# Performance work log

Measured on AMD Instinct MI355X. Metric: run time of the kernel, lower is better.

## Reference

```python
import jax, jax.numpy as jnp
import numpy as np

IN_DIM = 3
OUT_DIM = 3
HIDDEN = [40, 40, 40, 40, 40, 40]
N_POINTS = 2_097_152


def _glorot(key, fan_in, fan_out):
    std = jnp.sqrt(2.0 / (fan_in + fan_out)).astype(jnp.float32)
    return jax.random.normal(key, (fan_in, fan_out), dtype=jnp.float32) * std


def setup_inputs() -> dict:
    key = jax.random.key(0)
    keys = jax.random.split(key, 8)
    coords = jax.random.uniform(keys[0], (N_POINTS, IN_DIM), dtype=jnp.float32)
    dims = [IN_DIM] + HIDDEN + [OUT_DIM]  # [3,40,40,40,40,40,40,3]
    inp = {"coords": coords}
    for i in range(7):
        inp[f"W{i}"] = _glorot(keys[i + 1], dims[i], dims[i + 1])
        inp[f"b{i}"] = jnp.zeros((dims[i + 1],), dtype=jnp.float32)
    return inp


def reference(coords, W0, b0, W1, b1, W2, b2, W3, b3, W4, b4, W5, b5, W6, b6):
    # 7-layer coordinate MLP: Linear+Tanh x6, final Linear. coords: [N,3] -> [N,3]
    Ws = [W0, W1, W2, W3, W4, W5, W6]
    bs = [b0, b1, b2, b3, b4, b5, b6]
    x = coords
    for i in range(6):
        x = jnp.tanh(x @ Ws[i] + bs[i])
    return x @ Ws[6] + bs[6]
```

## Files before the change

kernel.cpp:

```cpp
#include <hip/hip_runtime.h>


typedef _Float16 f16x8 __attribute__((ext_vector_type(8)));
typedef float    f32x16 __attribute__((ext_vector_type(16)));
typedef unsigned int u32x4 __attribute__((ext_vector_type(4)));

#define NFRAG  35
#define TABN   385
#define TABREP 8
#define TABH   0.025f
#define INVH   40.0f
#define TABR   4.8f
#define UOFF   192.0f
#define UMAX   383.999f

__constant__ int INV[48] = {
     0,  1,  2,  3,   8,  9, 10, 11,   4,  5,  6,  7,  12, 13, 14, 15,
    16, 17, 18, 19,  24, 25, 26, 27,  20, 21, 22, 23,  28, 29, 30, 31,
    32, 33, 34, 35,  -1, -1, -1, -1,  36, 37, 38, 39,  -2, -3, -1, -1 };

__global__ void prep_frags(const float* __restrict__ W0, const float* __restrict__ b0,
                           const float* __restrict__ W1, const float* __restrict__ b1,
                           const float* __restrict__ W2, const float* __restrict__ b2,
                           const float* __restrict__ W3, const float* __restrict__ b3,
                           const float* __restrict__ W4, const float* __restrict__ b4,
                           const float* __restrict__ W5, const float* __restrict__ b5,
                           const float* __restrict__ W6, const float* __restrict__ b6,
                           unsigned short* __restrict__ frags,
                           float2* __restrict__ table)
{
    int tid = blockIdx.x * 256 + threadIdx.x;

    if (tid < NFRAG * 64) {
        int frag = tid >> 6, lane = tid & 63;

        int layer, mt, ch;
        if (frag < 2)       { layer = 0; mt = frag; ch = 0; }
        else if (frag < 32) { int t = frag - 2; layer = 1 + t / 6; int r = t % 6; mt = r / 3; ch = r % 3; }
        else                { layer = 6; mt = 0; ch = frag - 32; }

        const float* Ws[7] = { W0, W1, W2, W3, W4, W5, W6 };
        const float* bs[7] = { b0, b1, b2, b3, b4, b5, b6 };
        const float* W = Ws[layer];
        const float* b = bs[layer];
        const int fout = (layer == 6) ? 3 : 40;
        const float scale = (layer == 6) ? 1.0f : INVH;

        int jout  = mt * 32 + (lane & 31);
        int kbase = ch * 16 + (lane >> 5) * 8;

        unsigned short h[8];
        for (int i = 0; i < 8; ++i) {
            int k = kbase + i;
            float v = 0.0f;
            if (jout < fout) {
                int jin;
                if (layer == 0) jin = (k < 3) ? k : ((k == 3) ? -2 : ((k == 4) ? -3 : -1));
                else            jin = INV[k];
                if (jin >= 0)       v = W[jin * fout + jout] * scale;
                else if (jin == -2) v = b[jout] * scale;
                else if (jin == -3) v = (layer == 6) ? 0.0f : UOFF;
            }
            _Float16 hv = (_Float16)v;
            h[i] = __builtin_bit_cast(unsigned short, hv);
        }
        unsigned short* dst = frags + frag * 512 + lane * 8;
        for (int i = 0; i < 8; ++i) dst[i] = h[i];
    }
    else if (tid < NFRAG * 64 + TABN) {
        int i = tid - NFRAG * 64;
        float x  = -TABR + (float)i * TABH;
        float t0 = tanhf(x);
        float t1 = tanhf(x + TABH);
        float2 e = make_float2(t0, t1 - t0);
        for (int r = 0; r < TABREP; ++r) table[i * TABREP + r] = e;
    }
}

__device__ __forceinline__ unsigned int pkf16(float a, float b) {
    return __builtin_bit_cast(unsigned int, __builtin_amdgcn_cvt_pkrtz(a, b));
}
__device__ __forceinline__ f32x16 zf() {
    f32x16 v;
    #pragma unroll
    for (int i = 0; i < 16; ++i) v[i] = 0.0f;
    return v;
}

#define MFMA __builtin_amdgcn_mfma_f32_32x32x16_f16

#define ACT(Da, Db) do {                              \
    Bf[0]  = pkf16(tl(Da[0]),  tl(Da[1]));            \
    Bf[1]  = pkf16(tl(Da[2]),  tl(Da[3]));            \
    Bf[2]  = pkf16(tl(Da[4]),  tl(Da[5]));            \
    Bf[3]  = pkf16(tl(Da[6]),  tl(Da[7]));            \
    Bf[4]  = pkf16(tl(Da[8]),  tl(Da[9]));            \
    Bf[5]  = pkf16(tl(Da[10]), tl(Da[11]));           \
    Bf[6]  = pkf16(tl(Da[12]), tl(Da[13]));           \
    Bf[7]  = pkf16(tl(Da[14]), tl(Da[15]));           \
    Bf[8]  = pkf16(tl(Db[0]),  tl(Db[1]));            \
    Bf[9]  = pkf16(tl(Db[2]),  tl(Db[3]));            \
    Bf[10] = PK11;                                    \
    Bf[11] = 0u;                                      \
} while (0)

__global__ __launch_bounds__(512) void mlp_mfma(const float* __restrict__ coords,
                                                const unsigned short* __restrict__ frags,
                                                const float2* __restrict__ gtab,
                                                float* __restrict__ out, int npts)
{
    __shared__ __align__(16) unsigned short sf[NFRAG * 512];
    __shared__ __align__(16) float2 stab[TABN * TABREP];
    {
        const u32x4* s1 = (const u32x4*)frags; u32x4* d1 = (u32x4*)sf;
        for (int i = threadIdx.x; i < NFRAG * 64; i += 512) d1[i] = s1[i];
        const u32x4* s2 = (const u32x4*)gtab;  u32x4* d2 = (u32x4*)stab;
        for (int i = threadIdx.x; i < TABN * TABREP / 2; i += 512) d2[i] = s2[i];
    }
    __syncthreads();

    const int lane = threadIdx.x & 63;
    const int wid  = threadIdx.x >> 6;
    const int p    = (blockIdx.x * 8 + wid) * 32 + (lane & 31);
    const bool valid = (p < npts);

    float c0 = 0.f, c1 = 0.f, c2 = 0.f;
    if (valid) { c0 = coords[p * 3]; c1 = coords[p * 3 + 1]; c2 = coords[p * 3 + 2]; }

    const unsigned int PK11 = pkf16(1.0f, 1.0f);
    const float2* __restrict__ tb = stab + (lane & (TABREP - 1));
    const f32x16 CZ = zf();

    auto tl = [&](float u) -> float {
        u = __builtin_amdgcn_fmed3f(u, 0.0f, UMAX);
        float fr = __builtin_amdgcn_fractf(u);
        unsigned idx = (unsigned)u;
        float2 e = tb[idx * TABREP];
        return __builtin_fmaf(fr, e.y, e.x);
    };

    unsigned int Bf[12];
    Bf[0] = pkf16(c0, c1);
    Bf[1] = pkf16(c2, 1.0f);
    Bf[2] = pkf16(1.0f, 0.0f);
    Bf[3] = 0u;

    auto AF = [&](int f) -> f16x8 {
        return ((const f16x8*)sf)[f * 64 + lane];
    };
    auto BF = [&](int c) -> f16x8 {
        u32x4 t = { Bf[4 * c + 0], Bf[4 * c + 1], Bf[4 * c + 2], Bf[4 * c + 3] };
        return __builtin_bit_cast(f16x8, t);
    };

    {
        f16x8 bb = BF(0);
        f32x16 D0 = MFMA(AF(0), bb, CZ, 0, 0, 0);
        f32x16 D1 = MFMA(AF(1), bb, CZ, 0, 0, 0);
        ACT(D0, D1);
    }

    #pragma unroll
    for (int l = 1; l <= 5; ++l) {
        const int fb = 2 + (l - 1) * 6;
        f16x8 bc0 = BF(0), bc1 = BF(1), bc2 = BF(2);
        f32x16 D0 = MFMA(AF(fb + 0), bc0, CZ, 0, 0, 0);
        D0 = MFMA(AF(fb + 1), bc1, D0, 0, 0, 0);
        D0 = MFMA(AF(fb + 2), bc2, D0, 0, 0, 0);
        f32x16 D1 = MFMA(AF(fb + 3), bc0, CZ, 0, 0, 0);
        D1 = MFMA(AF(fb + 4), bc1, D1, 0, 0, 0);
        D1 = MFMA(AF(fb + 5), bc2, D1, 0, 0, 0);
        ACT(D0, D1);
    }

    {
        f32x16 D0 = MFMA(AF(32), BF(0), CZ, 0, 0, 0);
        D0 = MFMA(AF(33), BF(1), D0, 0, 0, 0);
        D0 = MFMA(AF(34), BF(2), D0, 0, 0, 0);
        if (lane < 32 && valid) {
            out[p * 3 + 0] = D0[0];
            out[p * 3 + 1] = D0[1];
            out[p * 3 + 2] = D0[2];
        }
    }
}

extern "C" void kernel_launch(void* const* d_in, const int* in_sizes, int n_in,
                              void* d_out, int out_size, void* d_ws, size_t ws_size,
                              hipStream_t stream)
{
    const float* coords = (const float*)d_in[0];
    const float* W0 = (const float*)d_in[1];  const float* b0 = (const float*)d_in[2];
    const float* W1 = (const float*)d_in[3];  const float* b1 = (const float*)d_in[4];
    const float* W2 = (const float*)d_in[5];  const float* b2 = (const float*)d_in[6];
    const float* W3 = (const float*)d_in[7];  const float* b3 = (const float*)d_in[8];
    const float* W4 = (const float*)d_in[9];  const float* b4 = (const float*)d_in[10];
    const float* W5 = (const float*)d_in[11]; const float* b5 = (const float*)d_in[12];
    const float* W6 = (const float*)d_in[13]; const float* b6 = (const float*)d_in[14];
    float* out = (float*)d_out;

    unsigned short* frags = (unsigned short*)d_ws;
    float2* table = (float2*)((char*)d_ws + NFRAG * 1024);

    const int npts = in_sizes[0] / 3;

    const int prep_threads = NFRAG * 64 + TABN;
    prep_frags<<<(prep_threads + 255) / 256, 256, 0, stream>>>(
        W0, b0, W1, b1, W2, b2, W3, b3, W4, b4, W5, b5, W6, b6, frags, table);

    const int blocks = (npts + 255) / 256;
    mlp_mfma<<<blocks, 512, 0, stream>>>(coords, frags, table, out, npts);
}
```

Measured before the change: 121.0 us.

## Pack tanh table entries as fp16 pairs and use fma_mix for interpolation

Table entries now store the tanh value and its slope as two packed fp16 halves in one 32-bit word instead of a float2. Interpolation uses v_fma_mixlo/mixhi, which writes fp16 results straight into the packed B operand, so the separate cvt_pkrtz packing step goes away. This halves LDS read width per lookup. The halved entry size pays for doubling the replication factor to 16 to reduce bank conflicts. Launch bounds now request 4 blocks per CU. The cost is lower precision in the table values and slopes.

```diff
diff --git a/kernel.cpp b/kernel.cpp
--- a/kernel.cpp
+++ b/kernel.cpp
@@ -7,7 +7,7 @@
 
 #define NFRAG  35
 #define TABN   385
-#define TABREP 8
+#define TABREP 16
 #define TABH   0.025f
 #define INVH   40.0f
 #define TABR   4.8f
@@ -27,7 +27,7 @@
                            const float* __restrict__ W5, const float* __restrict__ b5,
                            const float* __restrict__ W6, const float* __restrict__ b6,
                            unsigned short* __restrict__ frags,
-                           float2* __restrict__ table)
+                           unsigned* __restrict__ table)
 {
     int tid = blockIdx.x * 256 + threadIdx.x;
 
@@ -72,7 +72,9 @@
         float x  = -TABR + (float)i * TABH;
         float t0 = tanhf(x);
         float t1 = tanhf(x + TABH);
-        float2 e = make_float2(t0, t1 - t0);
+        unsigned short bb = __builtin_bit_cast(unsigned short, (_Float16)t0);
+        unsigned short dd = __builtin_bit_cast(unsigned short, (_Float16)(t1 - t0));
+        unsigned e = (unsigned)bb | ((unsigned)dd << 16);
         for (int r = 0; r < TABREP; ++r) table[i * TABREP + r] = e;
     }
 }
@@ -90,32 +92,32 @@
 #define MFMA __builtin_amdgcn_mfma_f32_32x32x16_f16
 
 #define ACT(Da, Db) do {                              \
-    Bf[0]  = pkf16(tl(Da[0]),  tl(Da[1]));            \
-    Bf[1]  = pkf16(tl(Da[2]),  tl(Da[3]));            \
-    Bf[2]  = pkf16(tl(Da[4]),  tl(Da[5]));            \
-    Bf[3]  = pkf16(tl(Da[6]),  tl(Da[7]));            \
-    Bf[4]  = pkf16(tl(Da[8]),  tl(Da[9]));            \
-    Bf[5]  = pkf16(tl(Da[10]), tl(Da[11]));           \
-    Bf[6]  = pkf16(tl(Da[12]), tl(Da[13]));           \
-    Bf[7]  = pkf16(tl(Da[14]), tl(Da[15]));           \
-    Bf[8]  = pkf16(tl(Db[0]),  tl(Db[1]));            \
-    Bf[9]  = pkf16(tl(Db[2]),  tl(Db[3]));            \
+    Bf[0]  = tl2(Da[0],  Da[1]);                      \
+    Bf[1]  = tl2(Da[2],  Da[3]);                      \
+    Bf[2]  = tl2(Da[4],  Da[5]);                      \
+    Bf[3]  = tl2(Da[6],  Da[7]);                      \
+    Bf[4]  = tl2(Da[8],  Da[9]);                      \
+    Bf[5]  = tl2(Da[10], Da[11]);                     \
+    Bf[6]  = tl2(Da[12], Da[13]);                     \
+    Bf[7]  = tl2(Da[14], Da[15]);                     \
+    Bf[8]  = tl2(Db[0],  Db[1]);                      \
+    Bf[9]  = tl2(Db[2],  Db[3]);                      \
     Bf[10] = PK11;                                    \
     Bf[11] = 0u;                                      \
 } while (0)
 
-__global__ __launch_bounds__(512) void mlp_mfma(const float* __restrict__ coords,
-                                                const unsigned short* __restrict__ frags,
-                                                const float2* __restrict__ gtab,
-                                                float* __restrict__ out, int npts)
+__global__ __launch_bounds__(512, 4) void mlp_mfma(const float* __restrict__ coords,
+                                                   const unsigned short* __restrict__ frags,
+                                                   const unsigned* __restrict__ gtab,
+                                                   float* __restrict__ out, int npts)
 {
     __shared__ __align__(16) unsigned short sf[NFRAG * 512];
-    __shared__ __align__(16) float2 stab[TABN * TABREP];
+    __shared__ __align__(16) unsigned stab[TABN * TABREP];
     {
         const u32x4* s1 = (const u32x4*)frags; u32x4* d1 = (u32x4*)sf;
         for (int i = threadIdx.x; i < NFRAG * 64; i += 512) d1[i] = s1[i];
         const u32x4* s2 = (const u32x4*)gtab;  u32x4* d2 = (u32x4*)stab;
-        for (int i = threadIdx.x; i < TABN * TABREP / 2; i += 512) d2[i] = s2[i];
+        for (int i = threadIdx.x; i < TABN * TABREP / 4; i += 512) d2[i] = s2[i];
     }
     __syncthreads();
 
@@ -128,15 +130,22 @@
     if (valid) { c0 = coords[p * 3]; c1 = coords[p * 3 + 1]; c2 = coords[p * 3 + 2]; }
 
     const unsigned int PK11 = pkf16(1.0f, 1.0f);
-    const float2* __restrict__ tb = stab + (lane & (TABREP - 1));
+    const unsigned* __restrict__ tb = stab + (lane & (TABREP - 1));
     const f32x16 CZ = zf();
 
-    auto tl = [&](float u) -> float {
-        u = __builtin_amdgcn_fmed3f(u, 0.0f, UMAX);
-        float fr = __builtin_amdgcn_fractf(u);
-        unsigned idx = (unsigned)u;
-        float2 e = tb[idx * TABREP];
-        return __builtin_fmaf(fr, e.y, e.x);
+    auto tl2 = [&](float ua, float ub) -> unsigned {
+        ua = __builtin_amdgcn_fmed3f(ua, 0.0f, UMAX);
+        ub = __builtin_amdgcn_fmed3f(ub, 0.0f, UMAX);
+        float fa = __builtin_amdgcn_fractf(ua);
+        float fb = __builtin_amdgcn_fractf(ub);
+        unsigned ea = tb[(unsigned)ua * TABREP];
+        unsigned eb = tb[(unsigned)ub * TABREP];
+        unsigned r;
+        asm("v_fma_mixlo_f16 %0, %1, %2, %2 op_sel:[0,1,0] op_sel_hi:[0,1,1]"
+            : "=v"(r) : "v"(fa), "v"(ea));
+        asm("v_fma_mixhi_f16 %0, %1, %2, %2 op_sel:[0,1,0] op_sel_hi:[0,1,1]"
+            : "+v"(r) : "v"(fb), "v"(eb));
+        return r;
     };
 
     unsigned int Bf[12];
@@ -200,7 +209,7 @@
     float* out = (float*)d_out;
 
     unsigned short* frags = (unsigned short*)d_ws;
-    float2* table = (float2*)((char*)d_ws + NFRAG * 1024);
+    unsigned* table = (unsigned*)((char*)d_ws + NFRAG * 1024);
 
     const int npts = in_sizes[0] / 3;
 
```

Result: no change. 122.2 us (+1.0%).
